# Kernel optimization log

Hardware: AMD Instinct MI355X
Metric: run time of the kernel (lower is better)

Reference implementation:

```python
import jax, jax.numpy as jnp
import numpy as np

DIM = 1024
SEQ = 32768
BATCH = 1
MIN_ACTIVE = 0.01
MAX_ACTIVE = 0.1
KMAX = int(MAX_ACTIVE * DIM) + 1  # static upper bound on dynamic k (<= 102)
EPS = 1e-6


def setup_inputs() -> dict:
    key = jax.random.key(0)
    ks = jax.random.split(key, 7)
    h = DIM // 8
    s = 0.02
    return {
        "x": jax.random.normal(ks[0], (BATCH, SEQ, DIM), jnp.float32),
        # complexity_net: Linear(dim, dim//8) -> GELU -> Linear(dim//8, 1) -> Sigmoid
        "w1": jax.random.normal(ks[1], (DIM, h), jnp.float32) * s,
        "b1": jnp.zeros((h,), jnp.float32),
        "w2": jax.random.normal(ks[2], (h, 1), jnp.float32) * s,
        "b2": jnp.zeros((1,), jnp.float32),
        # gate_net: Linear(dim, dim)
        "wg": jax.random.normal(ks[3], (DIM, DIM), jnp.float32) * s,
        "bg": jnp.zeros((DIM,), jnp.float32),
        # running stats (eval mode: used for normalization, not updated)
        "running_mean": jax.random.normal(ks[4], (DIM,), jnp.float32) * 0.1,
        "running_var": jax.random.uniform(ks[5], (DIM,), jnp.float32, minval=0.5, maxval=1.5),
    }


def reference(x, w1, b1, w2, b2, wg, bg, running_mean, running_var):
    # complexity from seq-mean pooled features -> scalar in (0,1)
    pooled = x.mean(axis=1, keepdims=True)                      # (B,1,D)
    hid = jax.nn.gelu(pooled @ w1 + b1, approximate=False)      # torch GELU is exact erf
    complexity = jax.nn.sigmoid(hid @ w2 + b2)                  # (B,1,1)
    active_ratio = MIN_ACTIVE + (MAX_ACTIVE - MIN_ACTIVE) * complexity
    # torch .int() truncates; clamp(min=1). B==1 so k is effectively scalar.
    k = jnp.clip((active_ratio * DIM).astype(jnp.int32), 1, KMAX)  # (B,1,1)

    importance = jnp.abs(x @ wg + bg)                           # (B,S,D)
    importance = (importance - running_mean) / (jnp.sqrt(running_var) + EPS)

    # dynamic-k topk via static-KMAX top_k + threshold at the k-th largest value
    topk_vals, _ = jax.lax.top_k(importance, KMAX)              # (B,S,KMAX)
    idx = jnp.broadcast_to((k - 1).astype(jnp.int32), (x.shape[0], x.shape[1], 1))
    kth = jnp.take_along_axis(topk_vals, idx, axis=-1)          # (B,S,1)
    mask = (importance >= kth).astype(x.dtype)                  # (B,S,D), non-differentiable
    mask = jax.lax.stop_gradient(mask)

    # straight-through combine: forward = x*mask, backward passes grad to all of x
    sparse_x = x * mask + (x - jax.lax.stop_gradient(x)) * (1.0 - mask)

    complexity_mean = complexity.mean()
    active_ratio_mean = active_ratio.mean()
    active_neurons = k.astype(jnp.float32).mean()
    return sparse_x, complexity_mean, active_ratio_mean, active_neurons
```

## Files before the change

### kernel.cpp

```cpp
#include <hip/hip_runtime.h>
#include <cstdint>
#include <cstddef>

#define SEQ 32768
#define DIM 1024
#define HID 128
#define KMAXV 103

using f4 = __attribute__((ext_vector_type(4))) float;
using f2 = __attribute__((ext_vector_type(2))) float;

__global__ __launch_bounds__(256) void pool_partial(const float* __restrict__ x,
                                                    double* __restrict__ part) {
    const int b = blockIdx.x;
    const int t = threadIdx.x;
    const int r0 = b * 128;
    double s0 = 0.0, s1 = 0.0, s2 = 0.0, s3 = 0.0;
    for (int r = 0; r < 128; ++r) {
        const float* row = x + (size_t)(r0 + r) * DIM;
        s0 += (double)row[t];
        s1 += (double)row[t + 256];
        s2 += (double)row[t + 512];
        s3 += (double)row[t + 768];
    }
    double* p = part + (size_t)b * DIM;
    p[t] = s0; p[t + 256] = s1; p[t + 512] = s2; p[t + 768] = s3;
}

__global__ __launch_bounds__(1024) void tiny_net(const double* __restrict__ part,
                                                 const float* __restrict__ w1,
                                                 const float* __restrict__ b1,
                                                 const float* __restrict__ w2,
                                                 const float* __restrict__ b2,
                                                 float* __restrict__ out_scalars,
                                                 int* __restrict__ kout) {
    __shared__ double pooled[DIM];
    __shared__ double hidv[HID];
    const int t = threadIdx.x;

    double s = 0.0;
    for (int b = 0; b < 256; ++b) s += part[(size_t)b * DIM + t];
    pooled[t] = s / (double)SEQ;
    __syncthreads();

    if (t < HID) {
        double h = (double)b1[t];
        for (int d = 0; d < DIM; ++d) h += pooled[d] * (double)w1[d * HID + t];
        h = 0.5 * h * (1.0 + erf(h * 0.70710678118654752440));
        hidv[t] = h;
    }
    __syncthreads();

    if (t == 0) {
        double z = (double)b2[0];
        for (int j = 0; j < HID; ++j) z += hidv[j] * (double)w2[j];
        double c = 1.0 / (1.0 + exp(-z));
        double ar = 0.01 + 0.09 * c;
        int k = (int)(ar * (double)DIM);
        if (k < 1) k = 1;
        if (k > KMAXV) k = KMAXV;
        out_scalars[0] = (float)c;
        out_scalars[1] = (float)ar;
        out_scalars[2] = (float)k;
        *kout = k;
    }
}

#define BM 16
#define CBLOCK 512

__device__ __forceinline__ void fma_step4(const f4 xq[8],
                                          f4 w0, f4 w1, f4 w2, f4 w3,
                                          f2 acc[8][2]) {
    const f2 w0lo = __builtin_shufflevector(w0, w0, 0, 1);
    const f2 w0hi = __builtin_shufflevector(w0, w0, 2, 3);
    const f2 w1lo = __builtin_shufflevector(w1, w1, 0, 1);
    const f2 w1hi = __builtin_shufflevector(w1, w1, 2, 3);
    const f2 w2lo = __builtin_shufflevector(w2, w2, 0, 1);
    const f2 w2hi = __builtin_shufflevector(w2, w2, 2, 3);
    const f2 w3lo = __builtin_shufflevector(w3, w3, 0, 1);
    const f2 w3hi = __builtin_shufflevector(w3, w3, 2, 3);
#pragma unroll
    for (int m = 0; m < 8; ++m) {
        const f2 xab = __builtin_shufflevector(xq[m], xq[m], 0, 1);
        const f2 xcd = __builtin_shufflevector(xq[m], xq[m], 2, 3);
        asm("v_pk_fma_f32 %0, %1, %2, %0 op_sel:[0,0,0] op_sel_hi:[0,1,1]"
            : "+v"(acc[m][0]) : "s"(xab), "v"(w0lo));
        asm("v_pk_fma_f32 %0, %1, %2, %0 op_sel:[0,0,0] op_sel_hi:[0,1,1]"
            : "+v"(acc[m][1]) : "s"(xab), "v"(w0hi));
        asm("v_pk_fma_f32 %0, %1, %2, %0 op_sel:[1,0,0] op_sel_hi:[1,1,1]"
            : "+v"(acc[m][0]) : "s"(xab), "v"(w1lo));
        asm("v_pk_fma_f32 %0, %1, %2, %0 op_sel:[1,0,0] op_sel_hi:[1,1,1]"
            : "+v"(acc[m][1]) : "s"(xab), "v"(w1hi));
        asm("v_pk_fma_f32 %0, %1, %2, %0 op_sel:[0,0,0] op_sel_hi:[0,1,1]"
            : "+v"(acc[m][0]) : "s"(xcd), "v"(w2lo));
        asm("v_pk_fma_f32 %0, %1, %2, %0 op_sel:[0,0,0] op_sel_hi:[0,1,1]"
            : "+v"(acc[m][1]) : "s"(xcd), "v"(w2hi));
        asm("v_pk_fma_f32 %0, %1, %2, %0 op_sel:[1,0,0] op_sel_hi:[1,1,1]"
            : "+v"(acc[m][0]) : "s"(xcd), "v"(w3lo));
        asm("v_pk_fma_f32 %0, %1, %2, %0 op_sel:[1,0,0] op_sel_hi:[1,1,1]"
            : "+v"(acc[m][1]) : "s"(xcd), "v"(w3hi));
    }
}

template<int K0, int K1>
__device__ __forceinline__ void panel_acc4(const float* __restrict__ xbase,
                                           const float* __restrict__ wbase,
                                           f2 acc[8][2]) {
#pragma unroll
    for (int m = 0; m < 8; ++m) {
        acc[m][0][0] = 0.0f; acc[m][0][1] = 0.0f;
        acc[m][1][0] = 0.0f; acc[m][1][1] = 0.0f;
    }

    f4 xA[8], xB[8];

#pragma unroll
    for (int m = 0; m < 8; ++m) xA[m] = *(const f4*)(xbase + m * DIM + K0);
    f4 wA0 = *(const f4*)(wbase + (size_t)(K0 + 0) * DIM);
    f4 wA1 = *(const f4*)(wbase + (size_t)(K0 + 1) * DIM);
    f4 wA2 = *(const f4*)(wbase + (size_t)(K0 + 2) * DIM);
    f4 wA3 = *(const f4*)(wbase + (size_t)(K0 + 3) * DIM);

    for (int kk0 = K0; kk0 < K1; kk0 += 8) {
#pragma unroll
        for (int m = 0; m < 8; ++m) xB[m] = *(const f4*)(xbase + m * DIM + kk0 + 4);
        const f4 wB0 = *(const f4*)(wbase + (size_t)(kk0 + 4) * DIM);
        const f4 wB1 = *(const f4*)(wbase + (size_t)(kk0 + 5) * DIM);
        const f4 wB2 = *(const f4*)(wbase + (size_t)(kk0 + 6) * DIM);
        const f4 wB3 = *(const f4*)(wbase + (size_t)(kk0 + 7) * DIM);

        fma_step4(xA, wA0, wA1, wA2, wA3, acc);

        const int kn = (kk0 + 8 < K1) ? kk0 + 8 : K0;
#pragma unroll
        for (int m = 0; m < 8; ++m) xA[m] = *(const f4*)(xbase + m * DIM + kn);
        wA0 = *(const f4*)(wbase + (size_t)(kn + 0) * DIM);
        wA1 = *(const f4*)(wbase + (size_t)(kn + 1) * DIM);
        wA2 = *(const f4*)(wbase + (size_t)(kn + 2) * DIM);
        wA3 = *(const f4*)(wbase + (size_t)(kn + 3) * DIM);

        fma_step4(xB, wB0, wB1, wB2, wB3, acc);
    }
}

__device__ __forceinline__ f4 acc_to_f4(const f2 a[2]) {
    return __builtin_shufflevector(a[0], a[1], 0, 1, 2, 3);
}

__global__ __launch_bounds__(CBLOCK) void panel1_kernel(const float* __restrict__ x,
                                                        const float* __restrict__ wg,
                                                        float* __restrict__ out) {
    const int t = threadIdx.x;
    const int c4 = (t & 255) << 2;
    const int rg = __builtin_amdgcn_readfirstlane(t >> 8);
    const int row0 = blockIdx.x * BM + rg * 8;

    f2 acc[8][2];
    panel_acc4<0, 384>(x + (size_t)row0 * DIM, wg + c4, acc);

#pragma unroll
    for (int m = 0; m < 8; ++m)
        *(f4*)(out + (size_t)(row0 + m) * DIM + c4) = acc_to_f4(acc[m]);
}

__global__ __launch_bounds__(CBLOCK) void panel2_kernel(const float* __restrict__ x,
                                                        const float* __restrict__ wg,
                                                        float* __restrict__ out) {
    const int t = threadIdx.x;
    const int c4 = (t & 255) << 2;
    const int rg = __builtin_amdgcn_readfirstlane(t >> 8);
    const int row0 = blockIdx.x * BM + rg * 8;

    f2 acc[8][2];
    panel_acc4<384, 704>(x + (size_t)row0 * DIM, wg + c4, acc);

#pragma unroll
    for (int m = 0; m < 8; ++m) {
        float* op = out + (size_t)(row0 + m) * DIM + c4;
        f4 d = *(const f4*)op;
        const f4 p = acc_to_f4(acc[m]);
#pragma unroll
        for (int j = 0; j < 4; ++j) d[j] = d[j] + p[j];
        *(f4*)op = d;
    }
}

__global__ __launch_bounds__(CBLOCK) void panel3_kernel(const float* __restrict__ x,
                                                        const float* __restrict__ wg,
                                                        const float* __restrict__ bg,
                                                        const float* __restrict__ rm,
                                                        const float* __restrict__ rv,
                                                        const int* __restrict__ kptr,
                                                        float* __restrict__ out) {
    __shared__ float lbuf[8 * DIM];

    const int t = threadIdx.x;
    const int c4 = (t & 255) << 2;
    const int rg = __builtin_amdgcn_readfirstlane(t >> 8);
    const int row0 = blockIdx.x * BM + rg * 8;

    f2 acc[8][2];
    panel_acc4<704, 1024>(x + (size_t)row0 * DIM, wg + c4, acc);

    f4 dot[8];
#pragma unroll
    for (int m = 0; m < 8; ++m) {
        const f4 d = *(const f4*)(out + (size_t)(row0 + m) * DIM + c4);
        const f4 p = acc_to_f4(acc[m]);
#pragma unroll
        for (int j = 0; j < 4; ++j) dot[m][j] = d[j] + p[j];
    }

    const f4 vbg = *(const f4*)(bg + c4);
    const f4 vrm = *(const f4*)(rm + c4);
    const f4 vrv = *(const f4*)(rv + c4);
    f4 vden;
#pragma unroll
    for (int j = 0; j < 4; ++j) vden[j] = sqrtf(vrv[j]) + 1e-6f;

    f4 imp[8];
#pragma unroll
    for (int m = 0; m < 8; ++m)
#pragma unroll
        for (int j = 0; j < 4; ++j)
            imp[m][j] = (fabsf(dot[m][j] + vbg[j]) - vrm[j]) / vden[j];

    int kval = *kptr;
    if (kval < 1) kval = 1;
    if (kval > DIM) kval = DIM;

    float (*selbuf)[DIM] = (float (*)[DIM])lbuf;

    for (int ch = 0; ch < 2; ++ch) {
        __syncthreads();
        if (rg == ch) {
#pragma unroll
            for (int m = 0; m < 8; ++m)
                *(f4*)(&selbuf[m][c4]) = imp[m];
        }
        __syncthreads();

        const int w = t >> 6;
        const int l = t & 63;
        const size_t srow = (size_t)(blockIdx.x * BM + ch * 8 + w);

        unsigned keys[16];
#pragma unroll
        for (int j = 0; j < 4; ++j) {
            const f4 v = *(const f4*)(&selbuf[w][4 * l + 256 * j]);
#pragma unroll
            for (int i = 0; i < 4; ++i) {
                const unsigned u = __float_as_uint(v[i]);
                keys[j * 4 + i] = (u & 0x80000000u) ? ~u : (u | 0x80000000u);
            }
        }

        unsigned pref = 0u;
        for (int b = 31; b >= 0; --b) {
            const unsigned tt = pref | (1u << b);
            int cnt = 0;
#pragma unroll
            for (int j = 0; j < 16; ++j) cnt += (keys[j] >= tt) ? 1 : 0;
#pragma unroll
            for (int off = 32; off >= 1; off >>= 1) cnt += __shfl_xor(cnt, off, 64);
            if (cnt >= kval) pref = tt;
        }

        const float* xr = x + srow * DIM;
        float* orow = out + srow * DIM;
#pragma unroll
        for (int j = 0; j < 4; ++j) {
            const f4 xv = *(const f4*)(xr + 4 * l + 256 * j);
            f4 o;
#pragma unroll
            for (int i = 0; i < 4; ++i) o[i] = (keys[j * 4 + i] >= pref) ? xv[i] : 0.0f;
            *(f4*)(orow + 4 * l + 256 * j) = o;
        }
    }
}

extern "C" void kernel_launch(void* const* d_in, const int* in_sizes, int n_in,
                              void* d_out, int out_size, void* d_ws, size_t ws_size,
                              hipStream_t stream) {
    const float* x  = (const float*)d_in[0];
    const float* w1 = (const float*)d_in[1];
    const float* b1 = (const float*)d_in[2];
    const float* w2 = (const float*)d_in[3];
    const float* b2 = (const float*)d_in[4];
    const float* wg = (const float*)d_in[5];
    const float* bg = (const float*)d_in[6];
    const float* rm = (const float*)d_in[7];
    const float* rv = (const float*)d_in[8];
    float* out = (float*)d_out;

    double* part = (double*)d_ws;
    int* kptr = (int*)((char*)d_ws + (size_t)256 * DIM * sizeof(double));

    pool_partial<<<256, 256, 0, stream>>>(x, part);
    tiny_net<<<1, 1024, 0, stream>>>(part, w1, b1, w2, b2,
                                     out + (size_t)SEQ * DIM, kptr);
    panel1_kernel<<<SEQ / BM, CBLOCK, 0, stream>>>(x, wg, out);
    panel2_kernel<<<SEQ / BM, CBLOCK, 0, stream>>>(x, wg, out);
    panel3_kernel<<<SEQ / BM, CBLOCK, 0, stream>>>(x, wg, bg, rm, rv, kptr, out);
}
```

Measured before the change: 1.022 ms.

## Double row tile to 32 per block with 1024 threads, drop manual k-loop prefetch

Blocks grow from 16 rows and 512 threads to 32 rows and 1024 threads, with 4 column-waves per row group, so each block shares more wg reads through cache. The top-k selection stage now handles 16 rows per pass in a 64KB shared buffer. The hand-written double-buffered x/w register prefetch in the inner k loop is replaced by a simple loop that loads and then computes, leaving latency hiding to the compiler and wave occupancy. The risks are fewer resident blocks per CU and exposed load latency without the explicit prefetch.

```diff
diff --git a/kernel.cpp b/kernel.cpp
--- a/kernel.cpp
+++ b/kernel.cpp
@@ -66,8 +66,8 @@
     }
 }
 
-#define BM 16
-#define CBLOCK 512
+#define BM 32
+#define CBLOCK 1024
 
 __device__ __forceinline__ void fma_step4(const f4 xq[8],
                                           f4 w0, f4 w1, f4 w2, f4 w3,
@@ -113,34 +113,16 @@
         acc[m][1][0] = 0.0f; acc[m][1][1] = 0.0f;
     }
 
-    f4 xA[8], xB[8];
-
-#pragma unroll
-    for (int m = 0; m < 8; ++m) xA[m] = *(const f4*)(xbase + m * DIM + K0);
-    f4 wA0 = *(const f4*)(wbase + (size_t)(K0 + 0) * DIM);
-    f4 wA1 = *(const f4*)(wbase + (size_t)(K0 + 1) * DIM);
-    f4 wA2 = *(const f4*)(wbase + (size_t)(K0 + 2) * DIM);
-    f4 wA3 = *(const f4*)(wbase + (size_t)(K0 + 3) * DIM);
-
-    for (int kk0 = K0; kk0 < K1; kk0 += 8) {
-#pragma unroll
-        for (int m = 0; m < 8; ++m) xB[m] = *(const f4*)(xbase + m * DIM + kk0 + 4);
-        const f4 wB0 = *(const f4*)(wbase + (size_t)(kk0 + 4) * DIM);
-        const f4 wB1 = *(const f4*)(wbase + (size_t)(kk0 + 5) * DIM);
-        const f4 wB2 = *(const f4*)(wbase + (size_t)(kk0 + 6) * DIM);
-        const f4 wB3 = *(const f4*)(wbase + (size_t)(kk0 + 7) * DIM);
-
-        fma_step4(xA, wA0, wA1, wA2, wA3, acc);
-
-        const int kn = (kk0 + 8 < K1) ? kk0 + 8 : K0;
-#pragma unroll
-        for (int m = 0; m < 8; ++m) xA[m] = *(const f4*)(xbase + m * DIM + kn);
-        wA0 = *(const f4*)(wbase + (size_t)(kn + 0) * DIM);
-        wA1 = *(const f4*)(wbase + (size_t)(kn + 1) * DIM);
-        wA2 = *(const f4*)(wbase + (size_t)(kn + 2) * DIM);
-        wA3 = *(const f4*)(wbase + (size_t)(kn + 3) * DIM);
-
-        fma_step4(xB, wB0, wB1, wB2, wB3, acc);
+    for (int kk0 = K0; kk0 < K1; kk0 += 4) {
+        const f4 w0 = *(const f4*)(wbase + (size_t)(kk0 + 0) * DIM);
+        const f4 w1 = *(const f4*)(wbase + (size_t)(kk0 + 1) * DIM);
+        const f4 w2 = *(const f4*)(wbase + (size_t)(kk0 + 2) * DIM);
+        const f4 w3 = *(const f4*)(wbase + (size_t)(kk0 + 3) * DIM);
+        f4 xq[8];
+#pragma unroll
+        for (int m = 0; m < 8; ++m)
+            xq[m] = *(const f4*)(xbase + m * DIM + kk0);
+        fma_step4(xq, w0, w1, w2, w3, acc);
     }
 }
 
@@ -152,8 +134,11 @@
                                                         const float* __restrict__ wg,
                                                         float* __restrict__ out) {
     const int t = threadIdx.x;
-    const int c4 = (t & 255) << 2;
-    const int rg = __builtin_amdgcn_readfirstlane(t >> 8);
+    const int lane = t & 63;
+    const int wid = t >> 6;
+    const int cw = wid & 3;
+    const int rg = __builtin_amdgcn_readfirstlane(wid >> 2);
+    const int c4 = (cw << 8) + (lane << 2);
     const int row0 = blockIdx.x * BM + rg * 8;
 
     f2 acc[8][2];
@@ -168,8 +153,11 @@
                                                         const float* __restrict__ wg,
                                                         float* __restrict__ out) {
     const int t = threadIdx.x;
-    const int c4 = (t & 255) << 2;
-    const int rg = __builtin_amdgcn_readfirstlane(t >> 8);
+    const int lane = t & 63;
+    const int wid = t >> 6;
+    const int cw = wid & 3;
+    const int rg = __builtin_amdgcn_readfirstlane(wid >> 2);
+    const int c4 = (cw << 8) + (lane << 2);
     const int row0 = blockIdx.x * BM + rg * 8;
 
     f2 acc[8][2];
@@ -193,11 +181,14 @@
                                                         const float* __restrict__ rv,
                                                         const int* __restrict__ kptr,
                                                         float* __restrict__ out) {
-    __shared__ float lbuf[8 * DIM];
-
-    const int t = threadIdx.x;
-    const int c4 = (t & 255) << 2;
-    const int rg = __builtin_amdgcn_readfirstlane(t >> 8);
+    __shared__ float selbuf[16][DIM];
+
+    const int t = threadIdx.x;
+    const int lane = t & 63;
+    const int wid = t >> 6;
+    const int cw = wid & 3;
+    const int rg = __builtin_amdgcn_readfirstlane(wid >> 2);
+    const int c4 = (cw << 8) + (lane << 2);
     const int row0 = blockIdx.x * BM + rg * 8;
 
     f2 acc[8][2];
@@ -230,25 +221,21 @@
     if (kval < 1) kval = 1;
     if (kval > DIM) kval = DIM;
 
-    float (*selbuf)[DIM] = (float (*)[DIM])lbuf;
-
     for (int ch = 0; ch < 2; ++ch) {
         __syncthreads();
-        if (rg == ch) {
+        if ((rg >> 1) == ch) {
 #pragma unroll
             for (int m = 0; m < 8; ++m)
-                *(f4*)(&selbuf[m][c4]) = imp[m];
+                *(f4*)(&selbuf[(rg & 1) * 8 + m][c4]) = imp[m];
         }
         __syncthreads();
 
-        const int w = t >> 6;
-        const int l = t & 63;
-        const size_t srow = (size_t)(blockIdx.x * BM + ch * 8 + w);
+        const size_t srow = (size_t)(blockIdx.x * BM + ch * 16 + wid);
 
         unsigned keys[16];
 #pragma unroll
         for (int j = 0; j < 4; ++j) {
-            const f4 v = *(const f4*)(&selbuf[w][4 * l + 256 * j]);
+            const f4 v = *(const f4*)(&selbuf[wid][4 * lane + 256 * j]);
 #pragma unroll
             for (int i = 0; i < 4; ++i) {
                 const unsigned u = __float_as_uint(v[i]);
@@ -271,11 +258,11 @@
         float* orow = out + srow * DIM;
 #pragma unroll
         for (int j = 0; j < 4; ++j) {
-            const f4 xv = *(const f4*)(xr + 4 * l + 256 * j);
+            const f4 xv = *(const f4*)(xr + 4 * lane + 256 * j);
             f4 o;
 #pragma unroll
             for (int i = 0; i < 4; ++i) o[i] = (keys[j * 4 + i] >= pref) ? xv[i] : 0.0f;
-            *(f4*)(orow + 4 * l + 256 * j) = o;
+            *(f4*)(orow + 4 * lane + 256 * j) = o;
         }
     }
 }
```

Measured after the change: 1.055 ms. 1.03x slower.

## Retile panel1/panel2 to 16 rows x 2 columns per thread, load x just-in-time

Applied to the files above, without the earlier changes.

Panel1 and panel2 now give each thread 2 output columns across all 16 rows of the block, instead of 4 columns across 8 rows, and read x straight from memory inside the FMA step as scalar-broadcast pairs. Panel_acc4, still used by panel3, stops double-buffering x in registers and loads it just before each FMA step. The aim is to cut the weight traffic per row and the register pressure from the x prefetch buffers, which may raise occupancy. In exchange there are more, narrower loads of weights and outputs, and less latency hiding for the x loads.

```diff
diff --git a/kernel.cpp b/kernel.cpp
--- a/kernel.cpp
+++ b/kernel.cpp
@@ -69,6 +69,91 @@
 #define BM 16
 #define CBLOCK 512
 
+__device__ __forceinline__ void fma_step2(const float* __restrict__ xp,
+                                          f2 w0, f2 w1, f2 w2, f2 w3,
+                                          f2 acc[16]) {
+#pragma unroll
+    for (int m = 0; m < 16; ++m) {
+        const f2 xab = *(const f2*)(xp + m * DIM);
+        const f2 xcd = *(const f2*)(xp + m * DIM + 2);
+        asm("v_pk_fma_f32 %0, %1, %2, %0 op_sel:[0,0,0] op_sel_hi:[0,1,1]"
+            : "+v"(acc[m]) : "s"(xab), "v"(w0));
+        asm("v_pk_fma_f32 %0, %1, %2, %0 op_sel:[1,0,0] op_sel_hi:[1,1,1]"
+            : "+v"(acc[m]) : "s"(xab), "v"(w1));
+        asm("v_pk_fma_f32 %0, %1, %2, %0 op_sel:[0,0,0] op_sel_hi:[0,1,1]"
+            : "+v"(acc[m]) : "s"(xcd), "v"(w2));
+        asm("v_pk_fma_f32 %0, %1, %2, %0 op_sel:[1,0,0] op_sel_hi:[1,1,1]"
+            : "+v"(acc[m]) : "s"(xcd), "v"(w3));
+    }
+}
+
+template<int K0, int K1>
+__device__ __forceinline__ void panel_acc2(const float* __restrict__ xbase,
+                                           const float* __restrict__ wbase,
+                                           f2 acc[16]) {
+#pragma unroll
+    for (int m = 0; m < 16; ++m) { acc[m][0] = 0.0f; acc[m][1] = 0.0f; }
+
+    f2 a0 = *(const f2*)(wbase + (size_t)(K0 + 0) * DIM);
+    f2 a1 = *(const f2*)(wbase + (size_t)(K0 + 1) * DIM);
+    f2 a2 = *(const f2*)(wbase + (size_t)(K0 + 2) * DIM);
+    f2 a3 = *(const f2*)(wbase + (size_t)(K0 + 3) * DIM);
+
+    for (int kk0 = K0; kk0 < K1; kk0 += 8) {
+        const f2 b0 = *(const f2*)(wbase + (size_t)(kk0 + 4) * DIM);
+        const f2 b1 = *(const f2*)(wbase + (size_t)(kk0 + 5) * DIM);
+        const f2 b2v = *(const f2*)(wbase + (size_t)(kk0 + 6) * DIM);
+        const f2 b3 = *(const f2*)(wbase + (size_t)(kk0 + 7) * DIM);
+
+        fma_step2(xbase + kk0, a0, a1, a2, a3, acc);
+
+        const int kn = (kk0 + 8 < K1) ? kk0 + 8 : K0;
+        const f2 c0 = *(const f2*)(wbase + (size_t)(kn + 0) * DIM);
+        const f2 c1 = *(const f2*)(wbase + (size_t)(kn + 1) * DIM);
+        const f2 c2v = *(const f2*)(wbase + (size_t)(kn + 2) * DIM);
+        const f2 c3 = *(const f2*)(wbase + (size_t)(kn + 3) * DIM);
+
+        fma_step2(xbase + kk0 + 4, b0, b1, b2v, b3, acc);
+
+        a0 = c0; a1 = c1; a2 = c2v; a3 = c3;
+    }
+}
+
+__global__ __launch_bounds__(CBLOCK) void panel1_kernel(const float* __restrict__ x,
+                                                        const float* __restrict__ wg,
+                                                        float* __restrict__ out) {
+    const int t = threadIdx.x;
+    const int c2 = t << 1;
+    const int row0 = blockIdx.x * BM;
+
+    f2 pacc[16];
+    panel_acc2<0, 384>(x + (size_t)row0 * DIM, wg + c2, pacc);
+
+#pragma unroll
+    for (int m = 0; m < 16; ++m)
+        *(f2*)(out + (size_t)(row0 + m) * DIM + c2) = pacc[m];
+}
+
+__global__ __launch_bounds__(CBLOCK) void panel2_kernel(const float* __restrict__ x,
+                                                        const float* __restrict__ wg,
+                                                        float* __restrict__ out) {
+    const int t = threadIdx.x;
+    const int c2 = t << 1;
+    const int row0 = blockIdx.x * BM;
+
+    f2 pacc[16];
+    panel_acc2<384, 704>(x + (size_t)row0 * DIM, wg + c2, pacc);
+
+#pragma unroll
+    for (int m = 0; m < 16; ++m) {
+        float* op = out + (size_t)(row0 + m) * DIM + c2;
+        f2 d = *(const f2*)op;
+        d[0] = d[0] + pacc[m][0];
+        d[1] = d[1] + pacc[m][1];
+        *(f2*)op = d;
+    }
+}
+
 __device__ __forceinline__ void fma_step4(const f4 xq[8],
                                           f4 w0, f4 w1, f4 w2, f4 w3,
                                           f2 acc[8][2]) {
@@ -113,77 +198,38 @@
         acc[m][1][0] = 0.0f; acc[m][1][1] = 0.0f;
     }
 
-    f4 xA[8], xB[8];
-
-#pragma unroll
-    for (int m = 0; m < 8; ++m) xA[m] = *(const f4*)(xbase + m * DIM + K0);
     f4 wA0 = *(const f4*)(wbase + (size_t)(K0 + 0) * DIM);
     f4 wA1 = *(const f4*)(wbase + (size_t)(K0 + 1) * DIM);
     f4 wA2 = *(const f4*)(wbase + (size_t)(K0 + 2) * DIM);
     f4 wA3 = *(const f4*)(wbase + (size_t)(K0 + 3) * DIM);
 
     for (int kk0 = K0; kk0 < K1; kk0 += 8) {
-#pragma unroll
-        for (int m = 0; m < 8; ++m) xB[m] = *(const f4*)(xbase + m * DIM + kk0 + 4);
         const f4 wB0 = *(const f4*)(wbase + (size_t)(kk0 + 4) * DIM);
         const f4 wB1 = *(const f4*)(wbase + (size_t)(kk0 + 5) * DIM);
         const f4 wB2 = *(const f4*)(wbase + (size_t)(kk0 + 6) * DIM);
         const f4 wB3 = *(const f4*)(wbase + (size_t)(kk0 + 7) * DIM);
 
-        fma_step4(xA, wA0, wA1, wA2, wA3, acc);
+        f4 xq[8];
+#pragma unroll
+        for (int m = 0; m < 8; ++m)
+            xq[m] = *(const f4*)(xbase + m * DIM + kk0);
+        fma_step4(xq, wA0, wA1, wA2, wA3, acc);
 
         const int kn = (kk0 + 8 < K1) ? kk0 + 8 : K0;
-#pragma unroll
-        for (int m = 0; m < 8; ++m) xA[m] = *(const f4*)(xbase + m * DIM + kn);
         wA0 = *(const f4*)(wbase + (size_t)(kn + 0) * DIM);
         wA1 = *(const f4*)(wbase + (size_t)(kn + 1) * DIM);
         wA2 = *(const f4*)(wbase + (size_t)(kn + 2) * DIM);
         wA3 = *(const f4*)(wbase + (size_t)(kn + 3) * DIM);
 
-        fma_step4(xB, wB0, wB1, wB2, wB3, acc);
+#pragma unroll
+        for (int m = 0; m < 8; ++m)
+            xq[m] = *(const f4*)(xbase + m * DIM + kk0 + 4);
+        fma_step4(xq, wB0, wB1, wB2, wB3, acc);
     }
 }
 
 __device__ __forceinline__ f4 acc_to_f4(const f2 a[2]) {
     return __builtin_shufflevector(a[0], a[1], 0, 1, 2, 3);
-}
-
-__global__ __launch_bounds__(CBLOCK) void panel1_kernel(const float* __restrict__ x,
-                                                        const float* __restrict__ wg,
-                                                        float* __restrict__ out) {
-    const int t = threadIdx.x;
-    const int c4 = (t & 255) << 2;
-    const int rg = __builtin_amdgcn_readfirstlane(t >> 8);
-    const int row0 = blockIdx.x * BM + rg * 8;
-
-    f2 acc[8][2];
-    panel_acc4<0, 384>(x + (size_t)row0 * DIM, wg + c4, acc);
-
-#pragma unroll
-    for (int m = 0; m < 8; ++m)
-        *(f4*)(out + (size_t)(row0 + m) * DIM + c4) = acc_to_f4(acc[m]);
-}
-
-__global__ __launch_bounds__(CBLOCK) void panel2_kernel(const float* __restrict__ x,
-                                                        const float* __restrict__ wg,
-                                                        float* __restrict__ out) {
-    const int t = threadIdx.x;
-    const int c4 = (t & 255) << 2;
-    const int rg = __builtin_amdgcn_readfirstlane(t >> 8);
-    const int row0 = blockIdx.x * BM + rg * 8;
-
-    f2 acc[8][2];
-    panel_acc4<384, 704>(x + (size_t)row0 * DIM, wg + c4, acc);
-
-#pragma unroll
-    for (int m = 0; m < 8; ++m) {
-        float* op = out + (size_t)(row0 + m) * DIM + c4;
-        f4 d = *(const f4*)op;
-        const f4 p = acc_to_f4(acc[m]);
-#pragma unroll
-        for (int j = 0; j < 4; ++j) d[j] = d[j] + p[j];
-        *(f4*)op = d;
-    }
 }
 
 __global__ __launch_bounds__(CBLOCK) void panel3_kernel(const float* __restrict__ x,
```

New measurement: 988.3 us. -3.3%, faster.
